# Performance work log

Hardware: AMD Instinct MI355X
Metric: run time of the kernel (lower is better)

## Reference

```python
import jax, jax.numpy as jnp
import numpy as np

B, S, DM, H = 4, 4096, 1024, 16
HD = DM // H

def setup_inputs() -> dict:
    key = jax.random.key(0)
    ks = jax.random.split(key, 9)
    sc = 1.0 / np.sqrt(DM)
    return {
        "x": jax.random.normal(ks[0], (B, S, DM), dtype=jnp.float32),
        "Wq": jax.random.normal(ks[1], (DM, DM), dtype=jnp.float32) * sc,
        "bq": jnp.zeros((DM,), dtype=jnp.float32),
        "Wk": jax.random.normal(ks[2], (DM, DM), dtype=jnp.float32) * sc,
        "bk": jnp.zeros((DM,), dtype=jnp.float32),
        "Wv": jax.random.normal(ks[3], (DM, DM), dtype=jnp.float32) * sc,
        "bv": jnp.zeros((DM,), dtype=jnp.float32),
        "Wo": jax.random.normal(ks[4], (DM, DM), dtype=jnp.float32) * sc,
        "bo": jnp.zeros((DM,), dtype=jnp.float32),
    }

def _heads(t):
    # [B,S,DM] -> [B,H,S,HD]
    return t.reshape(B, S, H, HD).transpose(0, 2, 1, 3)

def reference(x, Wq, bq, Wk, bk, Wv, bv, Wo, bo):
    q = _heads(x @ Wq.T + bq)
    k = _heads(x @ Wk.T + bk)
    v = _heads(x @ Wv.T + bv)
    q = jax.nn.elu(q) + 1.0  # positive feature map
    k = jax.nn.elu(k) + 1.0
    # kv aggregation: [B,H,HD,HD]
    kv = jnp.einsum('bhsd,bhse->bhde', k, v)
    qkv = jnp.einsum('bhsd,bhde->bhse', q, kv)  # [B,H,S,HD]
    k_sum = k.sum(axis=2)  # [B,H,HD]
    normalizer = jnp.einsum('bhsd,bhd->bhs', q, k_sum) + 1e-6
    out = qkv / normalizer[..., None]
    out = out.transpose(0, 2, 1, 3).reshape(B, S, DM)
    return out @ Wo.T + bo  # dropout is identity in eval
```

## Files before the change

### kernel.cpp

```cpp
#include <hip/hip_runtime.h>
#include <math.h>

#define NROWS  16384
#define DMODEL 1024
#define NHEAD  16
#define HDIM   64
#define SEQ    4096
#define NBATCH 4
#define NBH    64
#define SCHUNK 16
#define W1     2097152u

typedef __attribute__((ext_vector_type(8))) short bf16x8;
typedef __attribute__((ext_vector_type(4))) float f32x4;

__device__ __forceinline__ unsigned short f2bf(float f) {
    unsigned u = __float_as_uint(f);
    u += 0x7FFFu + ((u >> 16) & 1u);
    return (unsigned short)(u >> 16);
}
__device__ __forceinline__ float bf2f(unsigned short h) {
    return __uint_as_float((unsigned)h << 16);
}

__device__ __forceinline__ void gload16(const void* g, void* l) {
    __builtin_amdgcn_global_load_lds(
        (const __attribute__((address_space(1))) unsigned int*)g,
        (__attribute__((address_space(3))) unsigned int*)l, 16, 0, 0);
}

__global__ __launch_bounds__(256)
void split_x(const float* __restrict__ a, unsigned short* __restrict__ dst)
{
    const int idx = blockIdx.x * 256 + threadIdx.x;
    const int row = idx >> 8;
    const int c4  = (idx & 255) * 4;
    const float4 v = ((const float4*)a)[idx];
    ushort4 H, L;
    H.x = f2bf(v.x); L.x = f2bf(v.x - bf2f(H.x));
    H.y = f2bf(v.y); L.y = f2bf(v.y - bf2f(H.y));
    H.z = f2bf(v.z); L.z = f2bf(v.z - bf2f(H.z));
    H.w = f2bf(v.w); L.w = f2bf(v.w - bf2f(H.w));
    *(ushort4*)&dst[(size_t)row * 2048 + c4]        = H;
    *(ushort4*)&dst[(size_t)row * 2048 + 1024 + c4] = L;
}

__global__ __launch_bounds__(256)
void split_w4(const float* __restrict__ a0, const float* __restrict__ a1,
              const float* __restrict__ a2, const float* __restrict__ a3,
              unsigned short* __restrict__ dst)
{
    const int y = blockIdx.y;
    const float* src = (y == 0) ? a0 : (y == 1) ? a1 : (y == 2) ? a2 : a3;
    unsigned short* d = dst + (size_t)y * W1;
    const int idx = blockIdx.x * 256 + threadIdx.x;
    const int row = idx >> 8;
    const int c4  = (idx & 255) * 4;
    const float4 v = ((const float4*)src)[idx];
    ushort4 H, L;
    H.x = f2bf(v.x); L.x = f2bf(v.x - bf2f(H.x));
    H.y = f2bf(v.y); L.y = f2bf(v.y - bf2f(H.y));
    H.z = f2bf(v.z); L.z = f2bf(v.z - bf2f(H.z));
    H.w = f2bf(v.w); L.w = f2bf(v.w - bf2f(H.w));
    *(ushort4*)&d[(size_t)row * 2048 + c4]        = H;
    *(ushort4*)&d[(size_t)row * 2048 + 1024 + c4] = L;
}

template<int ELU>
__global__ __launch_bounds__(512)
void gemm_c3(const unsigned short* __restrict__ A2, const unsigned short* __restrict__ W2,
             const float* __restrict__ bias, float* __restrict__ C)
{
    __shared__ unsigned short lds[65536];
    const int t    = threadIdx.x;
    const int lane = t & 63;
    const int wv   = t >> 6;
    const int wr   = wv >> 2;
    const int wcn  = wv & 3;

    const int bid  = blockIdx.x;
    const int swz  = ((bid & 7) << 5) | (bid >> 3);
    const int am0  = (swz >> 2) * 256;
    const int bn0  = (swz & 3) * 256;

    const int fr   = lane & 15;
    const int j0   = lane >> 4;
    const int fx   = lane & 7;
    const int srow8 = lane >> 3;
    const int sslot = (lane & 7) ^ srow8;

    f32x4 acc[8][4];
#pragma unroll
    for (int i = 0; i < 8; ++i)
#pragma unroll
        for (int j = 0; j < 4; ++j)
#pragma unroll
            for (int e = 0; e < 4; ++e) acc[i][j][e] = 0.f;

    auto stageQ = [&](int q, int kt, unsigned wbU) {
        const int k0 = kt * 64;
        const bool isA = (q < 2);
        const int kb  = isA ? ((k0 < 1024) ? k0 : k0 - 1024)
                            : ((k0 < 2048) ? k0 : k0 - 2048);
        const unsigned short* src = isA ? A2 : W2;
        const int rb0 = (isA ? am0 : bn0) + (q & 1) * 128;
        const unsigned ldsT = wbU + (isA ? 0u : 16384u) + (unsigned)((q & 1) * 128) * 64u;
#pragma unroll
        for (int c = 0; c < 2; ++c) {
            const int r = rb0 + wv * 16 + c * 8 + srow8;
            gload16(src + (size_t)r * 2048 + kb + sslot * 8,
                    (unsigned short*)&lds[ldsT + (unsigned)(wv * 16 + c * 8) * 64u]);
        }
    };

#pragma unroll
    for (int q = 0; q < 4; ++q) stageQ(q, 0, 0u);
    __syncthreads();

    for (int kt = 0; kt < 48; ++kt) {
        const unsigned rbU = (kt & 1) ? 32768u : 0u;
        const unsigned wbU = rbU ^ 32768u;
        const bool pf = (kt < 47);

        bf16x8 bfr[2][4];
#pragma unroll
        for (int p = 0; p < 4; ++p) {
            if (p == 0) {
#pragma unroll
                for (int h = 0; h < 2; ++h)
#pragma unroll
                    for (int j = 0; j < 4; ++j) {
                        const unsigned phys = (unsigned)((h * 4 + j0) ^ fx);
                        bfr[h][j] = *(const bf16x8*)&lds[rbU + 16384u +
                            (unsigned)(wcn * 64 + j * 16 + fr) * 64u + phys * 8u];
                    }
            }
            bf16x8 afr[2][2];
#pragma unroll
            for (int i2 = 0; i2 < 2; ++i2) {
                const unsigned ar = (unsigned)(wr * 128 + (p * 2 + i2) * 16 + fr);
#pragma unroll
                for (int h = 0; h < 2; ++h) {
                    const unsigned phys = (unsigned)((h * 4 + j0) ^ fx);
                    afr[i2][h] = *(const bf16x8*)&lds[rbU + ar * 64u + phys * 8u];
                }
            }
            if (pf) {
                if (p == 0) { stageQ(0, kt + 1, wbU); stageQ(1, kt + 1, wbU); }
                else if (p == 1) stageQ(2, kt + 1, wbU);
                else if (p == 2) stageQ(3, kt + 1, wbU);
            }
            __builtin_amdgcn_s_barrier();
            __builtin_amdgcn_s_setprio(1);
#pragma unroll
            for (int i2 = 0; i2 < 2; ++i2)
#pragma unroll
                for (int j = 0; j < 4; ++j)
#pragma unroll
                    for (int h = 0; h < 2; ++h)
                        acc[p * 2 + i2][j] = __builtin_amdgcn_mfma_f32_16x16x32_bf16(
                            afr[i2][h], bfr[h][j], acc[p * 2 + i2][j], 0, 0, 0);
            __builtin_amdgcn_s_setprio(0);
            if (p < 3) __builtin_amdgcn_s_barrier();
        }
        __syncthreads();
    }

    const int crow0 = am0 + wr * 128 + (lane >> 4) * 4;
    const int ccol0 = bn0 + wcn * 64 + fr;
#pragma unroll
    for (int j = 0; j < 4; ++j) {
        const int col = ccol0 + j * 16;
        const float bv = bias[col];
#pragma unroll
        for (int i = 0; i < 8; ++i) {
            const int row = crow0 + i * 16;
#pragma unroll
            for (int r = 0; r < 4; ++r) {
                float v = acc[i][j][r] + bv;
                if (ELU) v = (v > 0.f) ? (v + 1.f) : __expf(v);
                C[(size_t)(row + r) * DMODEL + col] = v;
            }
        }
    }
}

__global__ __launch_bounds__(512)
void kv_partial(const float* __restrict__ k, const float* __restrict__ v,
                float* __restrict__ kvp, float* __restrict__ ksp)
{
    __shared__ float Ks[32][64];
    __shared__ float Vs[32][64];
    const int t  = threadIdx.x;
    const int bh = blockIdx.x;
    const int b  = bh >> 4;
    const int h  = bh & 15;
    const int sc = blockIdx.y;
    const int d  = t & 63;
    const int e0 = (t >> 6) * 8;

    float acc[8];
#pragma unroll
    for (int j = 0; j < 8; ++j) acc[j] = 0.f;
    float ks = 0.f;

    const size_t rowbase = (size_t)b * SEQ;
    const int sbeg = sc * (SEQ / SCHUNK);
    const int send = sbeg + (SEQ / SCHUNK);
    const int lrow = t >> 4;
    const int lc4  = (t & 15) * 4;

    for (int s0 = sbeg; s0 < send; s0 += 32) {
        const size_t g = (rowbase + s0 + lrow) * DMODEL + h * HDIM + lc4;
        *(float4*)&Ks[lrow][lc4] = *(const float4*)&k[g];
        *(float4*)&Vs[lrow][lc4] = *(const float4*)&v[g];
        __syncthreads();
#pragma unroll 8
        for (int sp = 0; sp < 32; ++sp) {
            const float kd = Ks[sp][d];
            if (t < 64) ks += Ks[sp][t];
            const float4 v0 = *(const float4*)&Vs[sp][e0 + 0];
            const float4 v1 = *(const float4*)&Vs[sp][e0 + 4];
            acc[0] = fmaf(kd, v0.x, acc[0]);  acc[1] = fmaf(kd, v0.y, acc[1]);
            acc[2] = fmaf(kd, v0.z, acc[2]);  acc[3] = fmaf(kd, v0.w, acc[3]);
            acc[4] = fmaf(kd, v1.x, acc[4]);  acc[5] = fmaf(kd, v1.y, acc[5]);
            acc[6] = fmaf(kd, v1.z, acc[6]);  acc[7] = fmaf(kd, v1.w, acc[7]);
        }
        __syncthreads();
    }

    const size_t base = ((size_t)sc * NBH + bh) * HDIM;
    float4 o0; o0.x = acc[0]; o0.y = acc[1]; o0.z = acc[2]; o0.w = acc[3];
    float4 o1; o1.x = acc[4]; o1.y = acc[5]; o1.z = acc[6]; o1.w = acc[7];
    *(float4*)&kvp[(base + d) * HDIM + e0 + 0] = o0;
    *(float4*)&kvp[(base + d) * HDIM + e0 + 4] = o1;
    if (t < 64) ksp[base + t] = ks;
}

__global__ __launch_bounds__(256)
void kv_reduce(const float* __restrict__ kvp, const float* __restrict__ ksp,
               float* __restrict__ kv, float* __restrict__ ksum)
{
    const int i = blockIdx.x * 256 + threadIdx.x;
    const int NKV = NBH * HDIM * HDIM;
    if (i < NKV) {
        float s = 0.f;
#pragma unroll
        for (int c = 0; c < SCHUNK; ++c) s += kvp[(size_t)c * NKV + i];
        kv[i] = s;
    }
    if (i < NBH * HDIM) {
        float s = 0.f;
#pragma unroll
        for (int c = 0; c < SCHUNK; ++c) s += ksp[(size_t)c * NBH * HDIM + i];
        ksum[i] = s;
    }
}

__global__ __launch_bounds__(256)
void qkv_norm(const float* __restrict__ q, const float* __restrict__ kv,
              const float* __restrict__ ksum, unsigned short* __restrict__ att)
{
    __shared__ float Qs[64][68];
    __shared__ float KVs[64][64];
    __shared__ float kss[64];
    const int t  = threadIdx.x;
    const int s0 = blockIdx.x * 64;
    const int b  = blockIdx.y;
    const int h  = blockIdx.z;
    const int bh = b * NHEAD + h;

#pragma unroll
    for (int i = 0; i < 4; ++i) {
        const int idx = i * 256 + t;
        const int row = idx >> 4;
        const int c4  = (idx & 15) * 4;
        const float4 vq = *(const float4*)&q[((size_t)b * SEQ + s0 + row) * DMODEL + h * HDIM + c4];
        *(float4*)&Qs[row][c4] = vq;
        *(float4*)&((float*)KVs)[idx * 4] = *(const float4*)&kv[(size_t)bh * HDIM * HDIM + idx * 4];
    }
    if (t < 64) kss[t] = ksum[(size_t)bh * HDIM + t];
    __syncthreads();

    const int r  = t >> 2;
    const int e0 = (t & 3) * 16;
    float out[16];
#pragma unroll
    for (int j = 0; j < 16; ++j) out[j] = 0.f;
    float nrm = 0.f;

#pragma unroll 8
    for (int d = 0; d < 64; ++d) {
        const float qd = Qs[r][d];
        nrm = fmaf(qd, kss[d], nrm);
        const float4 k0 = *(const float4*)&KVs[d][e0 + 0];
        const float4 k1 = *(const float4*)&KVs[d][e0 + 4];
        const float4 k2 = *(const float4*)&KVs[d][e0 + 8];
        const float4 k3 = *(const float4*)&KVs[d][e0 + 12];
        out[0]  = fmaf(qd, k0.x, out[0]);  out[1]  = fmaf(qd, k0.y, out[1]);
        out[2]  = fmaf(qd, k0.z, out[2]);  out[3]  = fmaf(qd, k0.w, out[3]);
        out[4]  = fmaf(qd, k1.x, out[4]);  out[5]  = fmaf(qd, k1.y, out[5]);
        out[6]  = fmaf(qd, k1.z, out[6]);  out[7]  = fmaf(qd, k1.w, out[7]);
        out[8]  = fmaf(qd, k2.x, out[8]);  out[9]  = fmaf(qd, k2.y, out[9]);
        out[10] = fmaf(qd, k2.z, out[10]); out[11] = fmaf(qd, k2.w, out[11]);
        out[12] = fmaf(qd, k3.x, out[12]); out[13] = fmaf(qd, k3.y, out[13]);
        out[14] = fmaf(qd, k3.z, out[14]); out[15] = fmaf(qd, k3.w, out[15]);
    }

    const float inv = 1.f / (nrm + 1e-6f);
    const size_t gb = ((size_t)b * SEQ + s0 + r) * 2048 + h * HDIM + e0;
#pragma unroll
    for (int g4 = 0; g4 < 4; ++g4) {
        ushort4 H, L;
        const float v0 = out[g4*4+0] * inv;
        const float v1 = out[g4*4+1] * inv;
        const float v2 = out[g4*4+2] * inv;
        const float v3 = out[g4*4+3] * inv;
        H.x = f2bf(v0); L.x = f2bf(v0 - bf2f(H.x));
        H.y = f2bf(v1); L.y = f2bf(v1 - bf2f(H.y));
        H.z = f2bf(v2); L.z = f2bf(v2 - bf2f(H.z));
        H.w = f2bf(v3); L.w = f2bf(v3 - bf2f(H.w));
        *(ushort4*)&att[gb + g4 * 4]        = H;
        *(ushort4*)&att[gb + 1024 + g4 * 4] = L;
    }
}

extern "C" void kernel_launch(void* const* d_in, const int* in_sizes, int n_in,
                              void* d_out, int out_size, void* d_ws, size_t ws_size,
                              hipStream_t stream)
{
    const float* x  = (const float*)d_in[0];
    const float* Wq = (const float*)d_in[1];
    const float* bq = (const float*)d_in[2];
    const float* Wk = (const float*)d_in[3];
    const float* bk = (const float*)d_in[4];
    const float* Wv = (const float*)d_in[5];
    const float* bv = (const float*)d_in[6];
    const float* Wo = (const float*)d_in[7];
    const float* bo = (const float*)d_in[8];

    unsigned short* xs  = (unsigned short*)d_ws;
    unsigned short* wsp = xs + (size_t)NROWS * 2048;
    float* buf0 = (float*)(wsp + 4u * W1);
    float* kv   = buf0 + (size_t)NROWS * DMODEL;
    float* ksum = kv + NBH * HDIM * HDIM;
    float* kvp  = ksum + NBH * HDIM;
    float* ksp  = kvp + (size_t)SCHUNK * NBH * HDIM * HDIM;
    float* vbuf = (float*)d_out;

    const dim3 gg(256);

    split_w4<<<dim3(1024, 4), 256, 0, stream>>>(Wq, Wk, Wv, Wo, wsp);
    split_x<<<16384, 256, 0, stream>>>(x, xs);
    gemm_c3<1><<<gg, 512, 0, stream>>>(xs, wsp + 1u * W1, bk, buf0);
    gemm_c3<0><<<gg, 512, 0, stream>>>(xs, wsp + 2u * W1, bv, vbuf);
    kv_partial<<<dim3(NBH, SCHUNK), 512, 0, stream>>>(buf0, vbuf, kvp, ksp);
    kv_reduce<<<1024, 256, 0, stream>>>(kvp, ksp, kv, ksum);
    gemm_c3<1><<<gg, 512, 0, stream>>>(xs, wsp, bq, buf0);
    qkv_norm<<<dim3(SEQ / 64, NBATCH, NHEAD), 256, 0, stream>>>(buf0, kv, ksum, xs);
    gemm_c3<0><<<gg, 512, 0, stream>>>(xs, wsp + 3u * W1, bo, (float*)d_out);
}
```

Measured before the change: 522.8 us.

## Restructure GEMM mainloop into 4-stage K=32 pipeline with vmcnt-based waits

Replaces the double-buffered K=64 tile loop, which used multiple barriers per iteration, with a four-deep ring of K=32 LDS tiles. Three tiles are prefetched ahead, and explicit s_waitcnt vmcnt plus a single barrier gate each step. The LDS layout changes from an XOR swizzle to a 16-row fragment-native layout, so each lane reads its MFMA fragment directly. The aim is better overlap of global-to-LDS loads with MFMA work and less sync overhead, at the risk of LDS bank conflicts from dropping the swizzle and a fragile hand-counted vmcnt.

```diff
diff --git a/kernel.cpp b/kernel.cpp
--- a/kernel.cpp
+++ b/kernel.cpp
@@ -13,6 +13,10 @@
 
 typedef __attribute__((ext_vector_type(8))) short bf16x8;
 typedef __attribute__((ext_vector_type(4))) float f32x4;
+
+#define VMCNT(N) asm volatile("s_waitcnt vmcnt(" #N ")" ::: "memory")
+#define BAR() do { asm volatile("" ::: "memory"); __builtin_amdgcn_s_barrier(); \
+                   asm volatile("" ::: "memory"); } while (0)
 
 __device__ __forceinline__ unsigned short f2bf(float f) {
     unsigned u = __float_as_uint(f);
@@ -68,7 +72,7 @@
 
 template<int ELU>
 __global__ __launch_bounds__(512)
-void gemm_c3(const unsigned short* __restrict__ A2, const unsigned short* __restrict__ W2,
+void gemm_p3(const unsigned short* __restrict__ A2, const unsigned short* __restrict__ W2,
              const float* __restrict__ bias, float* __restrict__ C)
 {
     __shared__ unsigned short lds[65536];
@@ -85,9 +89,9 @@
 
     const int fr   = lane & 15;
     const int j0   = lane >> 4;
-    const int fx   = lane & 7;
-    const int srow8 = lane >> 3;
-    const int sslot = (lane & 7) ^ srow8;
+    const unsigned fro = (unsigned)(j0 * 128 + fr * 8);
+    const int srcr = lane & 15;
+    const int srcc = (lane >> 4) * 8;
 
     f32x4 acc[8][4];
 #pragma unroll
@@ -97,74 +101,50 @@
 #pragma unroll
             for (int e = 0; e < 4; ++e) acc[i][j][e] = 0.f;
 
-    auto stageQ = [&](int q, int kt, unsigned wbU) {
-        const int k0 = kt * 64;
-        const bool isA = (q < 2);
-        const int kb  = isA ? ((k0 < 1024) ? k0 : k0 - 1024)
-                            : ((k0 < 2048) ? k0 : k0 - 2048);
-        const unsigned short* src = isA ? A2 : W2;
-        const int rb0 = (isA ? am0 : bn0) + (q & 1) * 128;
-        const unsigned ldsT = wbU + (isA ? 0u : 16384u) + (unsigned)((q & 1) * 128) * 64u;
+    auto stage_tile = [&](int kt) {
+        const int k0  = kt * 32;
+        const int kbA = (k0 < 1024) ? k0 : k0 - 1024;
+        const int kbB = (k0 < 2048) ? k0 : k0 - 2048;
+        const unsigned wb = ((unsigned)kt & 3u) * 16384u;
 #pragma unroll
         for (int c = 0; c < 2; ++c) {
-            const int r = rb0 + wv * 16 + c * 8 + srow8;
-            gload16(src + (size_t)r * 2048 + kb + sslot * 8,
-                    (unsigned short*)&lds[ldsT + (unsigned)(wv * 16 + c * 8) * 64u]);
+            const int ch = wv * 2 + c;
+            gload16(A2 + (size_t)(am0 + ch * 16 + srcr) * 2048 + kbA + srcc,
+                    (unsigned short*)&lds[wb + (unsigned)ch * 512u]);
+            gload16(W2 + (size_t)(bn0 + ch * 16 + srcr) * 2048 + kbB + srcc,
+                    (unsigned short*)&lds[wb + 8192u + (unsigned)ch * 512u]);
         }
     };
 
-#pragma unroll
-    for (int q = 0; q < 4; ++q) stageQ(q, 0, 0u);
-    __syncthreads();
-
-    for (int kt = 0; kt < 48; ++kt) {
-        const unsigned rbU = (kt & 1) ? 32768u : 0u;
-        const unsigned wbU = rbU ^ 32768u;
-        const bool pf = (kt < 47);
-
-        bf16x8 bfr[2][4];
-#pragma unroll
-        for (int p = 0; p < 4; ++p) {
-            if (p == 0) {
-#pragma unroll
-                for (int h = 0; h < 2; ++h)
-#pragma unroll
-                    for (int j = 0; j < 4; ++j) {
-                        const unsigned phys = (unsigned)((h * 4 + j0) ^ fx);
-                        bfr[h][j] = *(const bf16x8*)&lds[rbU + 16384u +
-                            (unsigned)(wcn * 64 + j * 16 + fr) * 64u + phys * 8u];
-                    }
-            }
-            bf16x8 afr[2][2];
-#pragma unroll
-            for (int i2 = 0; i2 < 2; ++i2) {
-                const unsigned ar = (unsigned)(wr * 128 + (p * 2 + i2) * 16 + fr);
-#pragma unroll
-                for (int h = 0; h < 2; ++h) {
-                    const unsigned phys = (unsigned)((h * 4 + j0) ^ fx);
-                    afr[i2][h] = *(const bf16x8*)&lds[rbU + ar * 64u + phys * 8u];
-                }
-            }
-            if (pf) {
-                if (p == 0) { stageQ(0, kt + 1, wbU); stageQ(1, kt + 1, wbU); }
-                else if (p == 1) stageQ(2, kt + 1, wbU);
-                else if (p == 2) stageQ(3, kt + 1, wbU);
-            }
-            __builtin_amdgcn_s_barrier();
-            __builtin_amdgcn_s_setprio(1);
-#pragma unroll
-            for (int i2 = 0; i2 < 2; ++i2)
-#pragma unroll
-                for (int j = 0; j < 4; ++j)
-#pragma unroll
-                    for (int h = 0; h < 2; ++h)
-                        acc[p * 2 + i2][j] = __builtin_amdgcn_mfma_f32_16x16x32_bf16(
-                            afr[i2][h], bfr[h][j], acc[p * 2 + i2][j], 0, 0, 0);
-            __builtin_amdgcn_s_setprio(0);
-            if (p < 3) __builtin_amdgcn_s_barrier();
-        }
-        __syncthreads();
-    }
+    auto compute = [&](int kt) {
+        const unsigned rd = ((unsigned)kt & 3u) * 16384u;
+        bf16x8 a[8], b[4];
+#pragma unroll
+        for (int j = 0; j < 4; ++j)
+            b[j] = *(const bf16x8*)&lds[rd + 8192u + (unsigned)((wcn * 4 + j) * 512) + fro];
+#pragma unroll
+        for (int i = 0; i < 8; ++i)
+            a[i] = *(const bf16x8*)&lds[rd + (unsigned)((wr * 8 + i) * 512) + fro];
+        __builtin_amdgcn_s_setprio(1);
+#pragma unroll
+        for (int i = 0; i < 8; ++i)
+#pragma unroll
+            for (int j = 0; j < 4; ++j)
+                acc[i][j] = __builtin_amdgcn_mfma_f32_16x16x32_bf16(a[i], b[j], acc[i][j], 0, 0, 0);
+        __builtin_amdgcn_s_setprio(0);
+    };
+
+    stage_tile(0); stage_tile(1); stage_tile(2);
+
+    for (int kt = 0; kt < 93; ++kt) {
+        VMCNT(8);
+        BAR();
+        stage_tile(kt + 3);
+        compute(kt);
+    }
+    VMCNT(8); BAR(); compute(93);
+    VMCNT(4); BAR(); compute(94);
+    VMCNT(0); BAR(); compute(95);
 
     const int crow0 = am0 + wr * 128 + (lane >> 4) * 4;
     const int ccol0 = bn0 + wcn * 64 + fr;
@@ -352,11 +332,11 @@
 
     split_w4<<<dim3(1024, 4), 256, 0, stream>>>(Wq, Wk, Wv, Wo, wsp);
     split_x<<<16384, 256, 0, stream>>>(x, xs);
-    gemm_c3<1><<<gg, 512, 0, stream>>>(xs, wsp + 1u * W1, bk, buf0);
-    gemm_c3<0><<<gg, 512, 0, stream>>>(xs, wsp + 2u * W1, bv, vbuf);
+    gemm_p3<1><<<gg, 512, 0, stream>>>(xs, wsp + 1u * W1, bk, buf0);
+    gemm_p3<0><<<gg, 512, 0, stream>>>(xs, wsp + 2u * W1, bv, vbuf);
     kv_partial<<<dim3(NBH, SCHUNK), 512, 0, stream>>>(buf0, vbuf, kvp, ksp);
     kv_reduce<<<1024, 256, 0, stream>>>(kvp, ksp, kv, ksum);
-    gemm_c3<1><<<gg, 512, 0, stream>>>(xs, wsp, bq, buf0);
+    gemm_p3<1><<<gg, 512, 0, stream>>>(xs, wsp, bq, buf0);
     qkv_norm<<<dim3(SEQ / 64, NBATCH, NHEAD), 256, 0, stream>>>(buf0, kv, ksum, xs);
-    gemm_c3<0><<<gg, 512, 0, stream>>>(xs, wsp + 3u * W1, bo, (float*)d_out);
-}
+    gemm_p3<0><<<gg, 512, 0, stream>>>(xs, wsp + 3u * W1, bo, (float*)d_out);
+}
```

After: 560.9 us. 1.07x slower.
